# Kernel tuning notes

Hardware: AMD Instinct MI355X
Metric: run time of the kernel (lower is better)

The kernel has to match this reference:

```python
import math
import jax, jax.numpy as jnp
import numpy as np

B, T, C = 4, 8192, 1024
EPS = 1e-5
LAYER_ID, N_LAYERS = 0, 24


def setup_inputs() -> dict:
    key = jax.random.key(0)
    ks = jax.random.split(key, 6)
    x = jax.random.normal(ks[0], (B, T, C), dtype=jnp.float32)
    # time_decay / time_first initialized exactly as in the torch __init__
    ratio_1_to_almost0 = 1.0 - LAYER_ID / N_LAYERS
    h = np.arange(C, dtype=np.float64)
    time_decay = (-5.0 + 8.0 * (h / (C - 1)) ** (0.7 + 1.3 * ratio_1_to_almost0)).astype(np.float32)
    zigzag = (((np.arange(C) + 1) % 3) - 1).astype(np.float32) * 0.5
    time_first = (math.log(0.3) + zigzag).astype(np.float32)
    # nn.Linear(dim, dim, bias=False) weights, stored as (out, in)
    std = 0.02
    Wk = jax.random.normal(ks[1], (C, C), dtype=jnp.float32) * std
    Wv = jax.random.normal(ks[2], (C, C), dtype=jnp.float32) * std
    Wr = jax.random.normal(ks[3], (C, C), dtype=jnp.float32) * std
    Wo = jax.random.normal(ks[4], (C, C), dtype=jnp.float32) * std
    ln_w = jnp.ones((C,), dtype=jnp.float32)
    ln_b = jnp.zeros((C,), dtype=jnp.float32)
    return {
        "x": x,
        "time_decay": jnp.asarray(time_decay),
        "time_first": jnp.asarray(time_first),
        "Wk": Wk, "Wv": Wv, "Wr": Wr, "Wo": Wo,
        "ln_w": ln_w, "ln_b": ln_b,
    }


def reference(x, time_decay, time_first, Wk, Wv, Wr, Wo, ln_w, ln_b):
    # LayerNorm (ln_x)
    mu = jnp.mean(x, axis=-1, keepdims=True)
    var = jnp.mean(jnp.square(x - mu), axis=-1, keepdims=True)
    xx = (x - mu) * jax.lax.rsqrt(var + EPS) * ln_w + ln_b

    # k, v, r projections (nn.Linear: y = x @ W^T)
    k = jnp.einsum('btc,dc->btd', xx, Wk)
    v = jnp.einsum('btc,dc->btd', xx, Wv)
    r = jnp.einsum('btc,dc->btd', xx, Wr)

    td = -jnp.exp(time_decay)   # (C,)
    tf = jnp.exp(time_first)    # (C,)

    # In the original loop, position j is weighted exp(td * j) regardless of t,
    # so wkv_history[t] = sum_{j < t} exp(td*j) * k[j] * v[j]  (exclusive cumsum).
    tpos = jnp.arange(T, dtype=jnp.float32)[:, None]        # (T,1)
    w = jnp.exp(td[None, :] * tpos)                         # (T,C)
    kv = k * v * w[None]                                    # (B,T,C)
    hist = jnp.cumsum(kv, axis=1) - kv                      # exclusive cumsum
    wkv = hist + k * tf

    out = jax.nn.sigmoid(r) * wkv
    return jnp.einsum('btc,dc->btd', out, Wo)
```

## Files before the change

kernel.cpp:

```cpp
#include <hip/hip_runtime.h>
#include <stdint.h>

#define B_ 4
#define T_ 8192
#define C_ 1024
#define BT_ (B_*T_)
#define NSEG 64
#define SLEN (T_/NSEG)
#define EPS_ 1e-5f
#define NT_ 32

typedef __attribute__((ext_vector_type(8))) short short8;
typedef __attribute__((ext_vector_type(4))) float float4v;
typedef __attribute__((ext_vector_type(4))) unsigned short ushort4v;
typedef unsigned short u16;

__device__ __forceinline__ u16 f2bf(float f){
  union { float f; uint32_t u; } v; v.f = f;
  uint32_t r = v.u + 0x7FFFu + ((v.u >> 16) & 1u);
  return (u16)(r >> 16);
}
__device__ __forceinline__ float bf2f(u16 h){
  union { uint32_t u; float f; } v; v.u = ((uint32_t)h) << 16;
  return v.f;
}
__device__ __forceinline__ void gload16(const void* g, void* l){
  __builtin_amdgcn_global_load_lds((__attribute__((address_space(1))) void*)(void*)g,
                                   (__attribute__((address_space(3))) void*)l,
                                   16, 0, 0);
}

__global__ void castw_kernel(const float* __restrict__ in, u16* __restrict__ out){
  int i = blockIdx.x*blockDim.x + threadIdx.x;
  float4v v = ((const float4v*)in)[i];
  ushort4v o;
  o.x=f2bf(v.x); o.y=f2bf(v.y); o.z=f2bf(v.z); o.w=f2bf(v.w);
  ((ushort4v*)out)[i] = o;
}

__global__ __launch_bounds__(256) void ln_kernel(const float* __restrict__ x,
    const float* __restrict__ lw, const float* __restrict__ lb, u16* __restrict__ xxb)
{
  int row = blockIdx.x;
  int tid = threadIdx.x;
  float4v v = ((const float4v*)(x + (size_t)row*C_))[tid];
  float s1 = v.x+v.y+v.z+v.w;
  float s2 = v.x*v.x+v.y*v.y+v.z*v.z+v.w*v.w;
  #pragma unroll
  for (int off=32; off>0; off>>=1){
    s1 += __shfl_down(s1, off, 64);
    s2 += __shfl_down(s2, off, 64);
  }
  __shared__ float red1[4], red2[4];
  if ((tid&63)==0){ red1[tid>>6]=s1; red2[tid>>6]=s2; }
  __syncthreads();
  s1 = red1[0]+red1[1]+red1[2]+red1[3];
  s2 = red2[0]+red2[1]+red2[2]+red2[3];
  float mu = s1*(1.0f/C_);
  float rs = rsqrtf(s2*(1.0f/C_) - mu*mu + EPS_);
  float4v wv = ((const float4v*)lw)[tid];
  float4v bv = ((const float4v*)lb)[tid];
  ushort4v o;
  o.x = f2bf((v.x-mu)*rs*wv.x + bv.x);
  o.y = f2bf((v.y-mu)*rs*wv.y + bv.y);
  o.z = f2bf((v.z-mu)*rs*wv.z + bv.z);
  o.w = f2bf((v.w-mu)*rs*wv.w + bv.w);
  ((ushort4v*)(xxb + (size_t)row*C_))[tid] = o;
}

template<bool F32OUT>
__global__ __launch_bounds__(512, 2) void gemm_dp(const u16* __restrict__ A,
    const u16* __restrict__ Bw, void* __restrict__ C0, void* __restrict__ C1,
    void* __restrict__ C2, int chunk)
{
  __shared__ __align__(16) u16 As[3*256*32];
  __shared__ __align__(16) u16 Bs[3*256*32];

  const int tid  = threadIdx.x;
  const int lane = tid & 63;
  const int wid  = tid >> 6;
  const int wr   = wid >> 2;
  const int wc   = wid & 3;

  const int lin = blockIdx.x;
  const int wg  = (lin & 7)*chunk + (lin >> 3);
  const int bm  = wg & 127;
  const int bn  = wg >> 7;

  const char* Ab = (const char*)(A  + (size_t)bm*256*C_);
  const char* Bb = (const char*)(Bw + (size_t)bn*256*C_);

  const int grow0 = wid*16 + (lane>>2);
  const int gsrc  = (((lane&3) ^ ((lane>>3)&3)) << 4);
  const char* Abt = Ab + (size_t)grow0*2048 + gsrc;
  const char* Bbt = Bb + (size_t)grow0*2048 + gsrc;
  char* AsW = (char*)As + wid*1024;
  char* BsW = (char*)Bs + wid*1024;

  const int gph   = ((lane>>4) ^ ((lane>>1)&3)) & 3;
  const int aoffb = (wr*128 + (lane&15))*64 + gph*16;
  const int boffb = (wc*64  + (lane&15))*64 + gph*16;

  float4v acc[8][4];
  float4v zero = {0.f,0.f,0.f,0.f};
  #pragma unroll
  for (int i=0;i<8;++i)
    #pragma unroll
    for (int j=0;j<4;++j) acc[i][j]=zero;

  #pragma unroll
  for (int j=0;j<2;++j){
    gload16(Abt + (size_t)j*262144 + 0*64, AsW + 0*16384 + j*8192);
    gload16(Bbt + (size_t)j*262144 + 0*64, BsW + 0*16384 + j*8192);
  }
  #pragma unroll
  for (int j=0;j<2;++j){
    gload16(Abt + (size_t)j*262144 + 1*64, AsW + 1*16384 + j*8192);
    gload16(Bbt + (size_t)j*262144 + 1*64, BsW + 1*16384 + j*8192);
  }

  int rd = 0, st = 2;
  for (int kt=0; kt<NT_; ++kt){
    if (kt < NT_-1) { asm volatile("s_waitcnt vmcnt(4)" ::: "memory"); }
    else            { asm volatile("s_waitcnt vmcnt(0)" ::: "memory"); }
    __builtin_amdgcn_sched_barrier(0);
    __builtin_amdgcn_s_barrier();
    __builtin_amdgcn_sched_barrier(0);

    if (kt+2 < NT_){
      #pragma unroll
      for (int j=0;j<2;++j){
        gload16(Abt + (size_t)j*262144 + (size_t)(kt+2)*64, AsW + st*16384 + j*8192);
        gload16(Bbt + (size_t)j*262144 + (size_t)(kt+2)*64, BsW + st*16384 + j*8192);
      }
    }

    const char* Abuf = (const char*)As + rd*16384;
    const char* Bbuf = (const char*)Bs + rd*16384;
    short8 bfr[4];
    #pragma unroll
    for (int ni=0;ni<4;++ni)
      bfr[ni] = *(const short8*)(Bbuf + boffb + ni*1024);
    __builtin_amdgcn_s_setprio(1);
    #pragma unroll
    for (int mi=0;mi<8;++mi){
      short8 a = *(const short8*)(Abuf + aoffb + mi*1024);
      #pragma unroll
      for (int ni=0;ni<4;++ni)
        acc[mi][ni] = __builtin_amdgcn_mfma_f32_16x16x32_bf16(a, bfr[ni], acc[mi][ni], 0,0,0);
    }
    __builtin_amdgcn_s_setprio(0);
    asm volatile("s_waitcnt lgkmcnt(0)" ::: "memory");
    __builtin_amdgcn_sched_barrier(0);

    rd = (rd==2)?0:rd+1;
    st = (st==2)?0:st+1;
  }

  const int cl = lane & 15, rq = lane >> 4;
  const size_t rbase = (size_t)bm*256 + wr*128;
  const int sel = bn >> 2;
  const int c0 = (bn&3)*256 + wc*64;
  void* cb = (sel==0) ? C0 : ((sel==1) ? C1 : C2);
  #pragma unroll
  for (int mi=0;mi<8;++mi)
    #pragma unroll
    for (int ni=0;ni<4;++ni)
      #pragma unroll
      for (int j=0;j<4;++j){
        size_t rr = rbase + mi*16 + rq*4 + j;
        int    cc = c0 + ni*16 + cl;
        if constexpr (F32OUT) ((float*)cb)[rr*1024 + cc] = acc[mi][ni][j];
        else                  ((u16*)cb)[rr*1024 + cc]   = f2bf(acc[mi][ni][j]);
      }
}

__global__ __launch_bounds__(256) void wkv_pass1(const u16* __restrict__ kb,
    const u16* __restrict__ vb, const float* __restrict__ tdecay,
    float* __restrict__ segsum)
{
  int c   = blockIdx.x*256 + threadIdx.x;
  int seg = blockIdx.y, b = blockIdx.z;
  float td = -expf(tdecay[c]);
  float d  = expf(td);
  int t0   = seg*SLEN;
  float w  = expf(td * (float)t0);
  size_t base = ((size_t)b*T_ + t0)*C_ + c;
  float s = 0.f;
  for (int i=0;i<SLEN;++i){
    float kk = bf2f(kb[base + (size_t)i*C_]);
    float vv = bf2f(vb[base + (size_t)i*C_]);
    s += kk*vv*w;
    w *= d;
  }
  segsum[((size_t)b*NSEG + seg)*C_ + c] = s;
}

__global__ void wkv_pass2(const float* __restrict__ segsum, float* __restrict__ segoff){
  int idx = blockIdx.x*256 + threadIdx.x;
  int b = idx / C_, c = idx % C_;
  float run = 0.f;
  for (int s=0;s<NSEG;++s){
    size_t o = ((size_t)b*NSEG + s)*C_ + c;
    segoff[o] = run;
    run += segsum[o];
  }
}

__global__ __launch_bounds__(256) void wkv_pass3(const u16* __restrict__ kb,
    const u16* __restrict__ vb, const u16* __restrict__ rb,
    const float* __restrict__ tdecay, const float* __restrict__ tfirst,
    const float* __restrict__ segoff, u16* __restrict__ outb)
{
  int c   = blockIdx.x*256 + threadIdx.x;
  int seg = blockIdx.y, b = blockIdx.z;
  float td = -expf(tdecay[c]);
  float d  = expf(td);
  float tf = expf(tfirst[c]);
  int t0   = seg*SLEN;
  float w  = expf(td * (float)t0);
  float hist = segoff[((size_t)b*NSEG + seg)*C_ + c];
  size_t base = ((size_t)b*T_ + t0)*C_ + c;
  for (int i=0;i<SLEN;++i){
    float kk = bf2f(kb[base + (size_t)i*C_]);
    float vv = bf2f(vb[base + (size_t)i*C_]);
    float rr = bf2f(rb[base + (size_t)i*C_]);
    float wkv = hist + kk*tf;
    float sg  = 1.f/(1.f + expf(-rr));
    outb[base + (size_t)i*C_] = f2bf(sg*wkv);
    hist += kk*vv*w;
    w *= d;
  }
}

extern "C" void kernel_launch(void* const* d_in, const int* in_sizes, int n_in,
                              void* d_out, int out_size, void* d_ws, size_t ws_size,
                              hipStream_t stream)
{
  (void)in_sizes; (void)n_in; (void)out_size; (void)ws_size;
  const float* x   = (const float*)d_in[0];
  const float* tdc = (const float*)d_in[1];
  const float* tfc = (const float*)d_in[2];
  const float* Wk  = (const float*)d_in[3];
  const float* Wv  = (const float*)d_in[4];
  const float* Wr  = (const float*)d_in[5];
  const float* Wo  = (const float*)d_in[6];
  const float* lw  = (const float*)d_in[7];
  const float* lb  = (const float*)d_in[8];
  float* out = (float*)d_out;

  char* ws = (char*)d_ws;
  u16* xxb = (u16*)(ws);
  u16* rb  = (u16*)(ws + 67108864);
  u16* Wkb = (u16*)(ws + 134217728);
  u16* Wvb = (u16*)(ws + 136314880);
  u16* Wrb = (u16*)(ws + 138412032);
  u16* Wob = (u16*)(ws + 140509184);
  float* segsum = (float*)(ws + 142606336);
  float* segoff = (float*)(ws + 143654912);
  u16* kb = (u16*)d_out;
  u16* vb = kb + (size_t)BT_*C_;
  u16* outb = xxb;

  castw_kernel<<<1024,256,0,stream>>>(Wk, Wkb);
  castw_kernel<<<1024,256,0,stream>>>(Wv, Wvb);
  castw_kernel<<<1024,256,0,stream>>>(Wr, Wrb);
  castw_kernel<<<1024,256,0,stream>>>(Wo, Wob);

  ln_kernel<<<BT_,256,0,stream>>>(x, lw, lb, xxb);

  gemm_dp<false><<<1536,512,0,stream>>>(xxb, Wkb, kb, vb, rb, 192);

  dim3 sg(C_/256, NSEG, B_);
  wkv_pass1<<<sg,256,0,stream>>>(kb, vb, tdc, segsum);
  wkv_pass2<<<16,256,0,stream>>>(segsum, segoff);
  wkv_pass3<<<sg,256,0,stream>>>(kb, vb, rb, tdc, tfc, segoff, outb);

  gemm_dp<true><<<512,512,0,stream>>>(outb, Wob, out, out, out, 64);
}
```

Baseline: 536.4 us.

## Restructure GEMM mainloop to 64-wide K tiles with quadrant-interleaved LDS reads

The bf16 GEMM now uses 64-element K tiles (16 iterations instead of 32) with a double-buffered 128KB LDS layout. Within each tile, LDS fragment reads and MFMA quadrants are interleaved across barriers, and the next-stage global loads are issued mid-tile. The block-to-tile mapping also changes so each XCD-like group of 8 covers 16 M-blocks across all N-blocks, aiming for better L2 reuse. This adds more barriers per tile and raises LDS use to 128KB, which can reduce occupancy despite the declared launch bounds of 2.

After: 500.2 us. 1.07x faster.

```diff
diff --git a/kernel.cpp b/kernel.cpp
--- a/kernel.cpp
+++ b/kernel.cpp
@@ -8,7 +8,7 @@
 #define NSEG 64
 #define SLEN (T_/NSEG)
 #define EPS_ 1e-5f
-#define NT_ 32
+#define NT_ 16
 
 typedef __attribute__((ext_vector_type(8))) short short8;
 typedef __attribute__((ext_vector_type(4))) float float4v;
@@ -68,13 +68,34 @@
   ((ushort4v*)(xxb + (size_t)row*C_))[tid] = o;
 }
 
+#define SYNC() do{ __builtin_amdgcn_sched_barrier(0); __builtin_amdgcn_s_barrier(); __builtin_amdgcn_sched_barrier(0); }while(0)
+
+#define RD_A(DST, MH, BO) \
+  _Pragma("unroll") for (int mt=0; mt<4; ++mt) \
+    _Pragma("unroll") for (int ks=0; ks<2; ++ks) \
+      DST[mt*2+ks] = *(const short8*)(lds + (BO) + ks*16384 + aoff0 + ((MH)*4+mt)*1024);
+
+#define RD_B(DST, NH, BO) \
+  _Pragma("unroll") for (int nt=0; nt<2; ++nt) \
+    _Pragma("unroll") for (int ks=0; ks<2; ++ks) \
+      DST[nt*2+ks] = *(const short8*)(lds + (BO) + ks*16384 + boff0 + ((NH)*2+nt)*1024);
+
+#define MFMA_Q(AS, BS, MH, NH) do{ \
+  __builtin_amdgcn_s_setprio(1); \
+  _Pragma("unroll") for (int ks=0; ks<2; ++ks) \
+    _Pragma("unroll") for (int mt=0; mt<4; ++mt) \
+      _Pragma("unroll") for (int nt=0; nt<2; ++nt) \
+        acc[(MH)*4+mt][(NH)*2+nt] = __builtin_amdgcn_mfma_f32_16x16x32_bf16( \
+            AS[mt*2+ks], BS[nt*2+ks], acc[(MH)*4+mt][(NH)*2+nt], 0,0,0); \
+  __builtin_amdgcn_s_setprio(0); \
+}while(0)
+
 template<bool F32OUT>
 __global__ __launch_bounds__(512, 2) void gemm_dp(const u16* __restrict__ A,
     const u16* __restrict__ Bw, void* __restrict__ C0, void* __restrict__ C1,
-    void* __restrict__ C2, int chunk)
-{
-  __shared__ __align__(16) u16 As[3*256*32];
-  __shared__ __align__(16) u16 Bs[3*256*32];
+    void* __restrict__ C2, int nbn)
+{
+  __shared__ __align__(1024) char lds[131072];
 
   const int tid  = threadIdx.x;
   const int lane = tid & 63;
@@ -83,23 +104,23 @@
   const int wc   = wid & 3;
 
   const int lin = blockIdx.x;
-  const int wg  = (lin & 7)*chunk + (lin >> 3);
-  const int bm  = wg & 127;
-  const int bn  = wg >> 7;
-
-  const char* Ab = (const char*)(A  + (size_t)bm*256*C_);
-  const char* Bb = (const char*)(Bw + (size_t)bn*256*C_);
-
-  const int grow0 = wid*16 + (lane>>2);
-  const int gsrc  = (((lane&3) ^ ((lane>>3)&3)) << 4);
-  const char* Abt = Ab + (size_t)grow0*2048 + gsrc;
-  const char* Bbt = Bb + (size_t)grow0*2048 + gsrc;
-  char* AsW = (char*)As + wid*1024;
-  char* BsW = (char*)Bs + wid*1024;
-
-  const int gph   = ((lane>>4) ^ ((lane>>1)&3)) & 3;
-  const int aoffb = (wr*128 + (lane&15))*64 + gph*16;
-  const int boffb = (wc*64  + (lane&15))*64 + gph*16;
+  const int x   = lin & 7;
+  const int wl  = lin >> 3;
+  const int bm  = x*16 + wl / nbn;
+  const int bn  = wl % nbn;
+
+  const int l15   = lane & 15;
+  const int lswz  = ((lane>>4) ^ ((l15>>1)&3)) << 4;
+  const int aoff0 = (wr*128 + l15)*64 + lswz;
+  const int boff0 = 65536 + (wc*64 + l15)*64 + lswz;
+
+  const int kk   = wid >> 2;
+  const int rg0  = (wid & 3)*2;
+  const int kkL  = kk*16384;
+  const char* Asrc = ((const char*)A)  + ((size_t)bm*256 + (lane>>2))*2048
+                     + (((lane&3) ^ ((lane>>3)&3)) << 4) + kk*64;
+  const char* Bsrc = ((const char*)Bw) + ((size_t)bn*256 + (lane>>2))*2048
+                     + (((lane&3) ^ ((lane>>3)&3)) << 4) + kk*64;
 
   float4v acc[8][4];
   float4v zero = {0.f,0.f,0.f,0.f};
@@ -108,56 +129,57 @@
     #pragma unroll
     for (int j=0;j<4;++j) acc[i][j]=zero;
 
-  #pragma unroll
-  for (int j=0;j<2;++j){
-    gload16(Abt + (size_t)j*262144 + 0*64, AsW + 0*16384 + j*8192);
-    gload16(Bbt + (size_t)j*262144 + 0*64, BsW + 0*16384 + j*8192);
-  }
-  #pragma unroll
-  for (int j=0;j<2;++j){
-    gload16(Abt + (size_t)j*262144 + 1*64, AsW + 1*16384 + j*8192);
-    gload16(Bbt + (size_t)j*262144 + 1*64, BsW + 1*16384 + j*8192);
-  }
-
-  int rd = 0, st = 2;
-  for (int kt=0; kt<NT_; ++kt){
-    if (kt < NT_-1) { asm volatile("s_waitcnt vmcnt(4)" ::: "memory"); }
-    else            { asm volatile("s_waitcnt vmcnt(0)" ::: "memory"); }
-    __builtin_amdgcn_sched_barrier(0);
-    __builtin_amdgcn_s_barrier();
-    __builtin_amdgcn_sched_barrier(0);
-
-    if (kt+2 < NT_){
+  auto stage = [&](int bo, int ktB){
+    #pragma unroll
+    for (int h=0; h<2; ++h)
       #pragma unroll
-      for (int j=0;j<2;++j){
-        gload16(Abt + (size_t)j*262144 + (size_t)(kt+2)*64, AsW + st*16384 + j*8192);
-        gload16(Bbt + (size_t)j*262144 + (size_t)(kt+2)*64, BsW + st*16384 + j*8192);
+      for (int q=0; q<2; ++q){
+        const int rowoff = h*128 + (rg0+q)*16;
+        gload16(Asrc + (size_t)rowoff*2048 + ktB, lds + bo + kkL + rowoff*64);
+        gload16(Bsrc + (size_t)rowoff*2048 + ktB, lds + 65536 + bo + kkL + rowoff*64);
       }
-    }
-
-    const char* Abuf = (const char*)As + rd*16384;
-    const char* Bbuf = (const char*)Bs + rd*16384;
-    short8 bfr[4];
-    #pragma unroll
-    for (int ni=0;ni<4;++ni)
-      bfr[ni] = *(const short8*)(Bbuf + boffb + ni*1024);
-    __builtin_amdgcn_s_setprio(1);
-    #pragma unroll
-    for (int mi=0;mi<8;++mi){
-      short8 a = *(const short8*)(Abuf + aoffb + mi*1024);
-      #pragma unroll
-      for (int ni=0;ni<4;++ni)
-        acc[mi][ni] = __builtin_amdgcn_mfma_f32_16x16x32_bf16(a, bfr[ni], acc[mi][ni], 0,0,0);
-    }
-    __builtin_amdgcn_s_setprio(0);
-    asm volatile("s_waitcnt lgkmcnt(0)" ::: "memory");
-    __builtin_amdgcn_sched_barrier(0);
-
-    rd = (rd==2)?0:rd+1;
-    st = (st==2)?0:st+1;
-  }
-
-  const int cl = lane & 15, rq = lane >> 4;
+  };
+
+  stage(0, 0);
+  stage(32768, 128);
+  asm volatile("s_waitcnt vmcnt(8)" ::: "memory");
+  SYNC();
+
+  short8 A0r[8], A1r[8], B0r[4], B1r[4];
+
+  #define KTILE(KT, BO) do{ \
+     \
+    RD_A(A0r, 0, BO); RD_B(B0r, 0, BO); \
+    SYNC(); \
+    MFMA_Q(A0r, B0r, 0, 0); \
+    SYNC(); \
+     \
+    RD_A(A1r, 1, BO); \
+    SYNC(); \
+    MFMA_Q(A1r, B0r, 1, 0); \
+    SYNC(); \
+     \
+    RD_B(B1r, 1, BO); \
+    SYNC(); \
+    MFMA_Q(A1r, B1r, 1, 1); \
+    SYNC(); \
+     \
+    if ((KT) < NT_-2) stage(BO, ((KT)+2)*128); \
+    MFMA_Q(A0r, B1r, 0, 1); \
+    if ((KT) < NT_-1){ \
+      if ((KT) < NT_-2) { asm volatile("s_waitcnt vmcnt(8)" ::: "memory"); } \
+      else              { asm volatile("s_waitcnt vmcnt(0)" ::: "memory"); } \
+      SYNC(); \
+    } \
+  }while(0)
+
+  for (int kt2=0; kt2<NT_; kt2+=2){
+    KTILE(kt2,   0);
+    KTILE(kt2+1, 32768);
+  }
+  #undef KTILE
+
+  const int cl = l15, rq = lane >> 4;
   const size_t rbase = (size_t)bm*256 + wr*128;
   const int sel = bn >> 2;
   const int c0 = (bn&3)*256 + wc*64;
@@ -269,12 +291,12 @@
 
   ln_kernel<<<BT_,256,0,stream>>>(x, lw, lb, xxb);
 
-  gemm_dp<false><<<1536,512,0,stream>>>(xxb, Wkb, kb, vb, rb, 192);
+  gemm_dp<false><<<1536,512,0,stream>>>(xxb, Wkb, kb, vb, rb, 12);
 
   dim3 sg(C_/256, NSEG, B_);
   wkv_pass1<<<sg,256,0,stream>>>(kb, vb, tdc, segsum);
   wkv_pass2<<<16,256,0,stream>>>(segsum, segoff);
   wkv_pass3<<<sg,256,0,stream>>>(kb, vb, rb, tdc, tfc, segoff, outb);
 
-  gemm_dp<true><<<512,512,0,stream>>>(outb, Wob, out, out, out, 64);
-}
+  gemm_dp<true><<<512,512,0,stream>>>(outb, Wob, out, out, out, 4);
+}
```
